# Performance work log

Hardware: AMD Instinct MI355X
Metric: run time of the kernel (lower is better)

Reference implementation:

```python
import jax, jax.numpy as jnp
import numpy as np

B, S, H, HEADS = 4, 4096, 256, 4
DH = H // HEADS
WINDOW = 16
N = B * S
EPS = 1e-5


def _build_edges():
    half = WINDOW // 2
    i = np.arange(S)
    offs = np.concatenate([np.arange(-half, 0), np.arange(1, half)])  # j in [i-half, i+half), j != i
    j = i[:, None] + offs[None, :]
    valid = (j >= 0) & (j < S)
    src_i = np.broadcast_to(i[:, None], j.shape)[valid]
    tgt_j = j[valid]
    w = (1.0 / (1.0 + np.abs(src_i - tgt_j))).astype(np.float32)
    boff = np.arange(B)[:, None] * S
    src = (boff + src_i[None, :]).reshape(-1).astype(np.int32)
    tgt = (boff + tgt_j[None, :]).reshape(-1).astype(np.int32)
    w = np.tile(w, B)
    return src, tgt, w


def setup_inputs() -> dict:
    key = jax.random.key(0)
    ks = jax.random.split(key, 8)
    src, tgt, w = _build_edges()
    sc = 0.02
    return {
        "hidden_states": jax.random.normal(ks[0], (B, S, H), jnp.float32),
        "Wc": jax.random.normal(ks[1], (H, H), jnp.float32) * sc,
        "bc": jnp.zeros((H,), jnp.float32),
        "Wa": jax.random.normal(ks[2], (H, H), jnp.float32) * sc,
        "a_src": jax.random.normal(ks[3], (HEADS, DH), jnp.float32) * sc,
        "a_tgt": jax.random.normal(ks[4], (HEADS, DH), jnp.float32) * sc,
        "ba": jnp.zeros((H,), jnp.float32),
        "ln_g": jnp.ones((H,), jnp.float32),
        "ln_b": jnp.zeros((H,), jnp.float32),
        "Wg": jax.random.normal(ks[5], (2 * H, H), jnp.float32) * sc,
        "bg": jnp.zeros((H,), jnp.float32),
        "Wp": jax.random.normal(ks[6], (H, H), jnp.float32) * sc,
        "bp": jnp.zeros((H,), jnp.float32),
        "edge_weights": jnp.asarray(w),
        "src": jnp.asarray(src),
        "tgt": jnp.asarray(tgt),
    }


def _ln(x, g, b):
    mu = jnp.mean(x, -1, keepdims=True)
    var = jnp.mean((x - mu) ** 2, -1, keepdims=True)
    return (x - mu) * jax.lax.rsqrt(var + EPS) * g + b


def reference(hidden_states, Wc, bc, Wa, a_src, a_tgt, ba, ln_g, ln_b,
              Wg, bg, Wp, bp, edge_weights, src, tgt):
    x = hidden_states.reshape(N, H)

    # --- layer 0: GraphConvolution ---
    support = x @ Wc                                   # [N,H]
    msg = edge_weights[:, None] * support[src]         # [E,H]
    gs = jax.ops.segment_sum(msg, tgt, num_segments=N) + bc
    gs = _ln(gs + x, ln_g, ln_b)

    # --- layer 1: GraphAttention (GAT-style, edge-weighted softmax) ---
    h = (gs @ Wa).reshape(N, HEADS, DH)
    es = jnp.einsum('nhd,hd->nh', h, a_src)            # [N,heads]
    et = jnp.einsum('nhd,hd->nh', h, a_tgt)
    logits = jax.nn.leaky_relu(es[src] + et[tgt], 0.2)  # [E,heads]
    m = jax.ops.segment_max(logits, tgt, num_segments=N)
    un = jnp.exp(logits - m[tgt]) * edge_weights[:, None]
    den = jax.ops.segment_sum(un, tgt, num_segments=N)
    alpha = un / (den[tgt] + 1e-9)                      # [E,heads]
    agg = jax.ops.segment_sum(alpha[:, :, None] * h[src], tgt, num_segments=N)
    gs = agg.reshape(N, H) + ba
    gs = _ln(gs + x, ln_g, ln_b)

    # --- gated integration ---
    gate = jax.nn.sigmoid(jnp.concatenate([x, gs], -1) @ Wg + bg)
    enhanced = x + gate * (gs @ Wp + bp)
    return enhanced.reshape(B, S, H)
```

## Files before the change

kernel.cpp:

```cpp
#include <hip/hip_runtime.h>
#include <math.h>

#define HD 256
#define SEQ 4096
#define NR 16384
#define NHEADS 4
#define EPSV 1e-5f
#define LDP 72
#define ZLDP 264
#define SROWS 32
#define SHALO 15
#define SLDP 264

typedef __attribute__((ext_vector_type(8))) short bf16x8;
typedef __attribute__((ext_vector_type(4))) float f32x4;

__device__ inline short f2bf(float f) {
    unsigned u = __float_as_uint(f);
    u += 0x7FFF + ((u >> 16) & 1);
    return (short)(u >> 16);
}
__device__ inline float bf2f(short s) {
    return __uint_as_float(((unsigned)(unsigned short)s) << 16);
}

__device__ inline void stage_w(const short* __restrict__ src, int src_stride,
                               int k0, short* lds)
{
    int t = threadIdx.x;
#pragma unroll
    for (int c = 0; c < 8; ++c) {
        int idx = c * 256 + t;
        int r = idx >> 3, kg = idx & 7;
        bf16x8 v = *(const bf16x8*)(src + (size_t)r * src_stride + k0 + kg * 8);
        *(bf16x8*)(lds + r * LDP + kg * 8) = v;
    }
}

__global__ __launch_bounds__(256) void prep_stencil(
    const float* __restrict__ x,
    const float* __restrict__ Wc, const float* __restrict__ Wa,
    const float* __restrict__ Wg, const float* __restrict__ Wp,
    short* __restrict__ xb, short* __restrict__ y,
    short* __restrict__ WcT, short* __restrict__ WaT,
    short* __restrict__ WgT, short* __restrict__ WpT)
{
    __shared__ __align__(16) char smem[(SROWS + SHALO) * SLDP * 2];
    int task = blockIdx.y;
    int bx = blockIdx.x;
    int t = threadIdx.x;

    if (task == 0) {
        short* lH = (short*)smem;
        int t0 = bx * SROWS;
        int batch_base = t0 & ~(SEQ - 1);
        for (int i = t; i < (SROWS + SHALO) * 64; i += 256) {
            int r = i >> 6, c4 = (i & 63) * 4;
            int grow = t0 - 7 + r;
            short4 o4 = {0, 0, 0, 0};
            if (grow >= batch_base && grow < batch_base + SEQ) {
                float4 v = *(const float4*)(x + (size_t)grow * HD + c4);
                o4.x = f2bf(v.x); o4.y = f2bf(v.y); o4.z = f2bf(v.z); o4.w = f2bf(v.w);
            }
            *(short4*)(lH + r * SLDP + c4) = o4;
        }
        __syncthreads();
        for (int i = t; i < SROWS * 64; i += 256) {
            int r = i >> 6, c4 = (i & 63) * 4;
            *(short4*)(xb + (size_t)(t0 + r) * HD + c4) =
                *(const short4*)(lH + (r + 7) * SLDP + c4);
        }
        int wv = t >> 6, lane = t & 63;
        int c0 = lane * 4;
        for (int rr = wv; rr < SROWS; rr += 4) {
            float a0 = 0.f, a1 = 0.f, a2 = 0.f, a3 = 0.f;
#pragma unroll
            for (int i = 0; i < 15; ++i) {
                int d = (i < 7) ? (i - 7) : (i - 6);
                float wd = 1.f / (1.f + (float)((d < 0) ? -d : d));
                short4 s4 = *(const short4*)(lH + (rr + 7 + d) * SLDP + c0);
                a0 += wd * bf2f(s4.x); a1 += wd * bf2f(s4.y);
                a2 += wd * bf2f(s4.z); a3 += wd * bf2f(s4.w);
            }
            short4 o;
            o.x = f2bf(a0); o.y = f2bf(a1); o.z = f2bf(a2); o.w = f2bf(a3);
            *(short4*)(y + (size_t)(t0 + rr) * HD + c0) = o;
        }
        return;
    }
    float (*lds)[65] = (float (*)[65])smem;
    const float* W; short* Wt; int K;
    if (task == 1)      { W = Wc; Wt = WcT; K = 256; }
    else if (task == 2) { W = Wa; Wt = WaT; K = 256; }
    else if (task == 3) { W = Wg; Wt = WgT; K = 512; }
    else                { W = Wp; Wt = WpT; K = 256; }
    int ntiles = (K >> 6) * 4;
    if (bx >= ntiles) return;
    int k0 = (bx >> 2) * 64, n0 = (bx & 3) * 64;
    int ty = t >> 6, tx = t & 63;
#pragma unroll
    for (int s = 0; s < 16; ++s) {
        int r = s * 4 + ty;
        lds[r][tx] = W[(size_t)(k0 + r) * 256 + n0 + tx];
    }
    __syncthreads();
#pragma unroll
    for (int s = 0; s < 16; ++s) {
        int rn = s * 4 + ty;
        Wt[(size_t)(n0 + rn) * K + k0 + tx] = f2bf(lds[tx][rn]);
    }
}

__global__ __launch_bounds__(256) void gemm_fused(
    const short* __restrict__ y, const short* __restrict__ WcT,
    const short* __restrict__ xb, const float* __restrict__ bc,
    const short* __restrict__ WaT,
    const float* __restrict__ lng, const float* __restrict__ lnb,
    const float* __restrict__ a_src, const float* __restrict__ a_tgt,
    short* __restrict__ hb, float* __restrict__ es, float* __restrict__ et)
{
    __shared__ __align__(16) short lB[256 * LDP];
    __shared__ __align__(16) short lZ[32 * ZLDP];
    __shared__ float red_s[64], red_q[64];
    int t = threadIdx.x;
    int m0 = blockIdx.x * SROWS;
    int lane = t & 63, wid = t >> 6;
    int wm = wid & 1, wn = wid >> 1;
    int lm = lane & 15, lk = (lane >> 4) * 8;
    int rbase = (lane >> 4) * 4;

#pragma unroll
    for (int c = 0; c < 4; ++c) {
        int idx = c * 256 + t;
        int r = idx >> 5, kg = idx & 31;
        *(bf16x8*)(lZ + r * ZLDP + kg * 8) =
            *(const bf16x8*)(y + (size_t)(m0 + r) * HD + kg * 8);
    }

    f32x4 acc[8] = {};
    for (int kt = 0; kt < 4; ++kt) {
        __syncthreads();
        stage_w(WcT, HD, kt * 64, lB);
        __syncthreads();
#pragma unroll
        for (int kk2 = 0; kk2 < 64; kk2 += 32) {
            bf16x8 a = *(const bf16x8*)(lZ + (wm * 16 + lm) * ZLDP + kt * 64 + kk2 + lk);
#pragma unroll
            for (int j = 0; j < 8; ++j) {
                bf16x8 b = *(const bf16x8*)(lB + (wn * 128 + j * 16 + lm) * LDP + kk2 + lk);
                acc[j] = __builtin_amdgcn_mfma_f32_16x16x32_bf16(a, b, acc[j], 0, 0, 0);
            }
        }
    }
    float zv[8][4];
    float s4r[4] = {}, q4r[4] = {};
#pragma unroll
    for (int j = 0; j < 8; ++j)
#pragma unroll
        for (int r = 0; r < 4; ++r) {
            int n = wn * 128 + j * 16 + lm;
            int row = m0 + wm * 16 + rbase + r;
            float z = acc[j][r] + bc[n] + bf2f(xb[(size_t)row * HD + n]);
            zv[j][r] = z; s4r[r] += z; q4r[r] += z * z;
        }
#pragma unroll
    for (int r = 0; r < 4; ++r)
#pragma unroll
        for (int o = 1; o < 16; o <<= 1) {
            s4r[r] += __shfl_xor(s4r[r], o, 64);
            q4r[r] += __shfl_xor(q4r[r], o, 64);
        }
    if (lm == 0)
#pragma unroll
        for (int r = 0; r < 4; ++r) {
            red_s[wn * 32 + wm * 16 + rbase + r] = s4r[r];
            red_q[wn * 32 + wm * 16 + rbase + r] = q4r[r];
        }
    __syncthreads();
    float mu[4], inv[4];
#pragma unroll
    for (int r = 0; r < 4; ++r) {
        int rowl = wm * 16 + rbase + r;
        float S = red_s[rowl] + red_s[32 + rowl];
        float Q = red_q[rowl] + red_q[32 + rowl];
        mu[r] = S * (1.f / HD);
        inv[r] = rsqrtf(Q * (1.f / HD) - mu[r] * mu[r] + EPSV);
    }
#pragma unroll
    for (int j = 0; j < 8; ++j)
#pragma unroll
        for (int r = 0; r < 4; ++r) {
            int n = wn * 128 + j * 16 + lm;
            int rowl = wm * 16 + rbase + r;
            lZ[rowl * ZLDP + n] = f2bf((zv[j][r] - mu[r]) * inv[r] * lng[n] + lnb[n]);
        }

    f32x4 acc2[8] = {};
    for (int kt = 0; kt < 4; ++kt) {
        __syncthreads();
        stage_w(WaT, HD, kt * 64, lB);
        __syncthreads();
#pragma unroll
        for (int kk2 = 0; kk2 < 64; kk2 += 32) {
            bf16x8 a = *(const bf16x8*)(lZ + (wm * 16 + lm) * ZLDP + kt * 64 + kk2 + lk);
#pragma unroll
            for (int j = 0; j < 8; ++j) {
                bf16x8 b = *(const bf16x8*)(lB + (wn * 128 + j * 16 + lm) * LDP + kk2 + lk);
                acc2[j] = __builtin_amdgcn_mfma_f32_16x16x32_bf16(a, b, acc2[j], 0, 0, 0);
            }
        }
    }
    float esA[4] = {}, etA[4] = {}, esB[4] = {}, etB[4] = {};
#pragma unroll
    for (int j = 0; j < 8; ++j) {
        int n = wn * 128 + j * 16 + lm;
        float as = a_src[n], at = a_tgt[n];
#pragma unroll
        for (int r = 0; r < 4; ++r) {
            int row = m0 + wm * 16 + rbase + r;
            hb[(size_t)row * HD + n] = f2bf(acc2[j][r]);
            if (j < 4) { esA[r] += acc2[j][r] * as; etA[r] += acc2[j][r] * at; }
            else       { esB[r] += acc2[j][r] * as; etB[r] += acc2[j][r] * at; }
        }
    }
#pragma unroll
    for (int r = 0; r < 4; ++r) {
#pragma unroll
        for (int o = 1; o < 16; o <<= 1) {
            esA[r] += __shfl_xor(esA[r], o, 64);
            etA[r] += __shfl_xor(etA[r], o, 64);
            esB[r] += __shfl_xor(esB[r], o, 64);
            etB[r] += __shfl_xor(etB[r], o, 64);
        }
        if (lm == 0) {
            int row = m0 + wm * 16 + rbase + r;
            es[row * NHEADS + wn * 2 + 0] = esA[r];
            et[row * NHEADS + wn * 2 + 0] = etA[r];
            es[row * NHEADS + wn * 2 + 1] = esB[r];
            et[row * NHEADS + wn * 2 + 1] = etB[r];
        }
    }
}

#define AF_LZ_OFF (256 * LDP * 2)
#define AF_LX_OFF (256 * LDP * 2 + 32 * ZLDP * 2)

__global__ __launch_bounds__(256) void attn_final(
    const short* __restrict__ hb, const float* __restrict__ es,
    const float* __restrict__ et, const short* __restrict__ xb,
    const float* __restrict__ ba, const float* __restrict__ lng,
    const float* __restrict__ lnb,
    const short* __restrict__ WgT, const float* __restrict__ bg,
    const short* __restrict__ WpT, const float* __restrict__ bp,
    float* __restrict__ out)
{
    __shared__ __align__(16) char smem[256 * LDP * 2 + 2 * 32 * ZLDP * 2];
    short* lH = (short*)smem;
    short* lB = (short*)smem;
    short* lZ = (short*)(smem + AF_LZ_OFF);
    short* lX = (short*)(smem + AF_LX_OFF);

    int t = threadIdx.x;
    int t0 = blockIdx.x * SROWS;
    int batch_base = t0 & ~(SEQ - 1);

    for (int i = t; i < (SROWS + SHALO) * 64; i += 256) {
        int r = i >> 6, c4 = (i & 63) * 4;
        int grow = t0 - 7 + r;
        short4 v = {0, 0, 0, 0};
        if (grow >= batch_base && grow < batch_base + SEQ)
            v = *(const short4*)(hb + (size_t)grow * HD + c4);
        *(short4*)(lH + r * SLDP + c4) = v;
    }
    for (int i = t; i < SROWS * 64; i += 256) {
        int r = i >> 6, c4 = (i & 63) * 4;
        *(short4*)(lX + r * ZLDP + c4) = *(const short4*)(xb + (size_t)(t0 + r) * HD + c4);
    }
    __syncthreads();

    int wv = t >> 6, lane = t & 63;
    int tap = lane >> 2, hh = lane & 3;
    int hd = lane >> 4;
    int c0 = lane * 4;
    for (int rr = wv; rr < SROWS; rr += 4) {
        int trow = t0 + rr;
        int p = trow & (SEQ - 1);
        float lg = -1e30f, wd = 0.f;
        bool okk = false;
        if (tap < 15) {
            int d = (tap < 7) ? (tap - 7) : (tap - 6);
            int qp = p + d;
            okk = (qp >= 0) && (qp < SEQ);
            if (okk) {
                float l = es[(trow + d) * NHEADS + hh] + et[trow * NHEADS + hh];
                lg = (l > 0.f) ? l : 0.2f * l;
            }
            wd = 1.f / (1.f + (float)((d < 0) ? -d : d));
        }
        float m = lg;
#pragma unroll
        for (int o = 4; o < 64; o <<= 1) m = fmaxf(m, __shfl_xor(m, o, 64));
        float un = okk ? __expf(lg - m) * wd : 0.f;
        float den = un;
#pragma unroll
        for (int o = 4; o < 64; o <<= 1) den += __shfl_xor(den, o, 64);
        float alpha_l = un / (den + 1e-9f);

        float al[15];
#pragma unroll
        for (int i = 0; i < 15; ++i) al[i] = __shfl(alpha_l, i * 4 + hd, 64);

        float a0 = 0.f, a1 = 0.f, a2 = 0.f, a3 = 0.f;
#pragma unroll
        for (int i = 0; i < 15; ++i) {
            int d = (i < 7) ? (i - 7) : (i - 6);
            short4 s4 = *(const short4*)(lH + (rr + 7 + d) * SLDP + c0);
            a0 += al[i] * bf2f(s4.x); a1 += al[i] * bf2f(s4.y);
            a2 += al[i] * bf2f(s4.z); a3 += al[i] * bf2f(s4.w);
        }
        short4 xv4 = *(const short4*)(lX + rr * ZLDP + c0);
        float4 bav = *(const float4*)(ba + c0);
        float v0 = a0 + bav.x + bf2f(xv4.x), v1 = a1 + bav.y + bf2f(xv4.y);
        float v2 = a2 + bav.z + bf2f(xv4.z), v3 = a3 + bav.w + bf2f(xv4.w);
        float s = v0 + v1 + v2 + v3;
        float q = v0 * v0 + v1 * v1 + v2 * v2 + v3 * v3;
#pragma unroll
        for (int o = 1; o < 64; o <<= 1) { s += __shfl_xor(s, o, 64); q += __shfl_xor(q, o, 64); }
        float mu = s * (1.f / HD);
        float var = q * (1.f / HD) - mu * mu;
        float inv = rsqrtf(var + EPSV);
        float4 gv = *(const float4*)(lng + c0);
        float4 bv = *(const float4*)(lnb + c0);
        short4 o4;
        o4.x = f2bf((v0 - mu) * inv * gv.x + bv.x);
        o4.y = f2bf((v1 - mu) * inv * gv.y + bv.y);
        o4.z = f2bf((v2 - mu) * inv * gv.z + bv.z);
        o4.w = f2bf((v3 - mu) * inv * gv.w + bv.w);
        *(short4*)(lZ + rr * ZLDP + c0) = o4;
    }

    int wid = t >> 6;
    int wm = wid & 1, wn = wid >> 1;
    int lm = lane & 15, lk = (lane >> 4) * 8;
    int rbase = (lane >> 4) * 4;
    f32x4 accg[8] = {}, accp[8] = {};
    for (int kt = 0; kt < 4; ++kt) {
        __syncthreads();
        stage_w(WgT, 512, kt * 64, lB);
        __syncthreads();
#pragma unroll
        for (int kk2 = 0; kk2 < 64; kk2 += 32) {
            bf16x8 a = *(const bf16x8*)(lX + (wm * 16 + lm) * ZLDP + kt * 64 + kk2 + lk);
#pragma unroll
            for (int j = 0; j < 8; ++j) {
                bf16x8 b = *(const bf16x8*)(lB + (wn * 128 + j * 16 + lm) * LDP + kk2 + lk);
                accg[j] = __builtin_amdgcn_mfma_f32_16x16x32_bf16(a, b, accg[j], 0, 0, 0);
            }
        }
    }
    for (int kt = 0; kt < 4; ++kt) {
        __syncthreads();
        stage_w(WgT, 512, 256 + kt * 64, lB);
        __syncthreads();
#pragma unroll
        for (int kk2 = 0; kk2 < 64; kk2 += 32) {
            bf16x8 a = *(const bf16x8*)(lZ + (wm * 16 + lm) * ZLDP + kt * 64 + kk2 + lk);
#pragma unroll
            for (int j = 0; j < 8; ++j) {
                bf16x8 b = *(const bf16x8*)(lB + (wn * 128 + j * 16 + lm) * LDP + kk2 + lk);
                accg[j] = __builtin_amdgcn_mfma_f32_16x16x32_bf16(a, b, accg[j], 0, 0, 0);
            }
        }
    }
    for (int kt = 0; kt < 4; ++kt) {
        __syncthreads();
        stage_w(WpT, HD, kt * 64, lB);
        __syncthreads();
#pragma unroll
        for (int kk2 = 0; kk2 < 64; kk2 += 32) {
            bf16x8 a = *(const bf16x8*)(lZ + (wm * 16 + lm) * ZLDP + kt * 64 + kk2 + lk);
#pragma unroll
            for (int j = 0; j < 8; ++j) {
                bf16x8 b = *(const bf16x8*)(lB + (wn * 128 + j * 16 + lm) * LDP + kk2 + lk);
                accp[j] = __builtin_amdgcn_mfma_f32_16x16x32_bf16(a, b, accp[j], 0, 0, 0);
            }
        }
    }
#pragma unroll
    for (int j = 0; j < 8; ++j)
#pragma unroll
        for (int r = 0; r < 4; ++r) {
            int n = wn * 128 + j * 16 + lm;
            int rowl = wm * 16 + rbase + r;
            size_t m = (size_t)(t0 + rowl);
            float gate = 1.f / (1.f + __expf(-(accg[j][r] + bg[n])));
            float pv = accp[j][r] + bp[n];
            out[m * HD + n] = bf2f(lX[rowl * ZLDP + n]) + gate * pv;
        }
}

extern "C" void kernel_launch(void* const* d_in, const int* in_sizes, int n_in,
                              void* d_out, int out_size, void* d_ws, size_t ws_size,
                              hipStream_t stream)
{
    const float* x     = (const float*)d_in[0];
    const float* Wc    = (const float*)d_in[1];
    const float* bc    = (const float*)d_in[2];
    const float* Wa    = (const float*)d_in[3];
    const float* a_src = (const float*)d_in[4];
    const float* a_tgt = (const float*)d_in[5];
    const float* ba    = (const float*)d_in[6];
    const float* ln_g  = (const float*)d_in[7];
    const float* ln_b  = (const float*)d_in[8];
    const float* Wg    = (const float*)d_in[9];
    const float* bg    = (const float*)d_in[10];
    const float* Wp    = (const float*)d_in[11];
    const float* bp    = (const float*)d_in[12];

    float* out = (float*)d_out;

    char* w = (char*)d_ws;
    short* y   = (short*)w;   w += (size_t)NR * HD * 2;
    short* xb  = (short*)w;   w += (size_t)NR * HD * 2;
    short* hb  = (short*)w;   w += (size_t)NR * HD * 2;
    float* es  = (float*)w;   w += (size_t)NR * NHEADS * 4;
    float* et  = (float*)w;   w += (size_t)NR * NHEADS * 4;
    short* WcT = (short*)w;   w += 256 * 256 * 2;
    short* WaT = (short*)w;   w += 256 * 256 * 2;
    short* WpT = (short*)w;   w += 256 * 256 * 2;
    short* WgT = (short*)w;   w += 512 * 256 * 2;

    prep_stencil<<<dim3(NR / SROWS, 5), 256, 0, stream>>>(
        x, Wc, Wa, Wg, Wp, xb, y, WcT, WaT, WgT, WpT);
    gemm_fused<<<NR / SROWS, 256, 0, stream>>>(y, WcT, xb, bc, WaT, ln_g, ln_b,
                                               a_src, a_tgt, hb, es, et);
    attn_final<<<NR / SROWS, 256, 0, stream>>>(hb, es, et, xb, ba, ln_g, ln_b,
                                               WgT, bg, WpT, bp, out);
}
```

Before: 67.54 us.

## Double-buffer weight tiles through registers with single barrier per k-step

Replaces the load-sync-compute-sync staging of weight tiles with a double-buffered pipeline over 32-wide k-slices. The next slice is prefetched into registers before the current MFMAs run, then stored to the alternate LDS buffer, so only one barrier is needed per step. Launch bounds gain occupancy hints (3 and 4 blocks per CU) to help hide latency. The costs are twice as many k-iterations, more registers held for the prefetch, and possible spilling under the tighter register limits.

```diff
diff --git a/kernel.cpp b/kernel.cpp
--- a/kernel.cpp
+++ b/kernel.cpp
@@ -6,7 +6,7 @@
 #define NR 16384
 #define NHEADS 4
 #define EPSV 1e-5f
-#define LDP 72
+#define LDP2 36
 #define ZLDP 264
 #define SROWS 32
 #define SHALO 15
@@ -24,16 +24,25 @@
     return __uint_as_float(((unsigned)(unsigned short)s) << 16);
 }
 
-__device__ inline void stage_w(const short* __restrict__ src, int src_stride,
-                               int k0, short* lds)
+__device__ inline void wload(const short* __restrict__ src, int src_stride,
+                             int k0, bf16x8 wreg[4])
 {
     int t = threadIdx.x;
 #pragma unroll
-    for (int c = 0; c < 8; ++c) {
+    for (int c = 0; c < 4; ++c) {
         int idx = c * 256 + t;
-        int r = idx >> 3, kg = idx & 7;
-        bf16x8 v = *(const bf16x8*)(src + (size_t)r * src_stride + k0 + kg * 8);
-        *(bf16x8*)(lds + r * LDP + kg * 8) = v;
+        int r = idx >> 2, kg = idx & 3;
+        wreg[c] = *(const bf16x8*)(src + (size_t)r * src_stride + k0 + kg * 8);
+    }
+}
+__device__ inline void wstore(short* lds, bf16x8 wreg[4])
+{
+    int t = threadIdx.x;
+#pragma unroll
+    for (int c = 0; c < 4; ++c) {
+        int idx = c * 256 + t;
+        int r = idx >> 2, kg = idx & 3;
+        *(bf16x8*)(lds + r * LDP2 + kg * 8) = wreg[c];
     }
 }
 
@@ -111,7 +120,7 @@
     }
 }
 
-__global__ __launch_bounds__(256) void gemm_fused(
+__global__ __launch_bounds__(256, 3) void gemm_fused(
     const short* __restrict__ y, const short* __restrict__ WcT,
     const short* __restrict__ xb, const float* __restrict__ bc,
     const short* __restrict__ WaT,
@@ -119,7 +128,7 @@
     const float* __restrict__ a_src, const float* __restrict__ a_tgt,
     short* __restrict__ hb, float* __restrict__ es, float* __restrict__ et)
 {
-    __shared__ __align__(16) short lB[256 * LDP];
+    __shared__ __align__(16) short lBp[2][256 * LDP2];
     __shared__ __align__(16) short lZ[32 * ZLDP];
     __shared__ float red_s[64], red_q[64];
     int t = threadIdx.x;
@@ -138,19 +147,25 @@
     }
 
     f32x4 acc[8] = {};
-    for (int kt = 0; kt < 4; ++kt) {
-        __syncthreads();
-        stage_w(WcT, HD, kt * 64, lB);
-        __syncthreads();
-#pragma unroll
-        for (int kk2 = 0; kk2 < 64; kk2 += 32) {
-            bf16x8 a = *(const bf16x8*)(lZ + (wm * 16 + lm) * ZLDP + kt * 64 + kk2 + lk);
-#pragma unroll
-            for (int j = 0; j < 8; ++j) {
-                bf16x8 b = *(const bf16x8*)(lB + (wn * 128 + j * 16 + lm) * LDP + kk2 + lk);
-                acc[j] = __builtin_amdgcn_mfma_f32_16x16x32_bf16(a, b, acc[j], 0, 0, 0);
-            }
-        }
+    {
+        bf16x8 w0[4];
+        wload(WcT, HD, 0, w0);
+        wstore(lBp[0], w0);
+    }
+    __syncthreads();
+    for (int kt = 0; kt < 8; ++kt) {
+        const short* cur = lBp[kt & 1];
+        short* nxt = (short*)lBp[(kt & 1) ^ 1];
+        bf16x8 wreg[4];
+        if (kt < 7) wload(WcT, HD, (kt + 1) * 32, wreg);
+        bf16x8 a = *(const bf16x8*)(lZ + (wm * 16 + lm) * ZLDP + kt * 32 + lk);
+#pragma unroll
+        for (int j = 0; j < 8; ++j) {
+            bf16x8 b = *(const bf16x8*)(cur + (wn * 128 + j * 16 + lm) * LDP2 + lk);
+            acc[j] = __builtin_amdgcn_mfma_f32_16x16x32_bf16(a, b, acc[j], 0, 0, 0);
+        }
+        if (kt < 7) wstore(nxt, wreg);
+        __syncthreads();
     }
     float zv[8][4];
     float s4r[4] = {}, q4r[4] = {};
@@ -194,21 +209,27 @@
             int rowl = wm * 16 + rbase + r;
             lZ[rowl * ZLDP + n] = f2bf((zv[j][r] - mu[r]) * inv[r] * lng[n] + lnb[n]);
         }
+    {
+        bf16x8 w0[4];
+        wload(WaT, HD, 0, w0);
+        wstore((short*)lBp[0], w0);
+    }
+    __syncthreads();
 
     f32x4 acc2[8] = {};
-    for (int kt = 0; kt < 4; ++kt) {
-        __syncthreads();
-        stage_w(WaT, HD, kt * 64, lB);
-        __syncthreads();
-#pragma unroll
-        for (int kk2 = 0; kk2 < 64; kk2 += 32) {
-            bf16x8 a = *(const bf16x8*)(lZ + (wm * 16 + lm) * ZLDP + kt * 64 + kk2 + lk);
-#pragma unroll
-            for (int j = 0; j < 8; ++j) {
-                bf16x8 b = *(const bf16x8*)(lB + (wn * 128 + j * 16 + lm) * LDP + kk2 + lk);
-                acc2[j] = __builtin_amdgcn_mfma_f32_16x16x32_bf16(a, b, acc2[j], 0, 0, 0);
-            }
-        }
+    for (int kt = 0; kt < 8; ++kt) {
+        const short* cur = lBp[kt & 1];
+        short* nxt = (short*)lBp[(kt & 1) ^ 1];
+        bf16x8 wreg[4];
+        if (kt < 7) wload(WaT, HD, (kt + 1) * 32, wreg);
+        bf16x8 a = *(const bf16x8*)(lZ + (wm * 16 + lm) * ZLDP + kt * 32 + lk);
+#pragma unroll
+        for (int j = 0; j < 8; ++j) {
+            bf16x8 b = *(const bf16x8*)(cur + (wn * 128 + j * 16 + lm) * LDP2 + lk);
+            acc2[j] = __builtin_amdgcn_mfma_f32_16x16x32_bf16(a, b, acc2[j], 0, 0, 0);
+        }
+        if (kt < 7) wstore(nxt, wreg);
+        __syncthreads();
     }
     float esA[4] = {}, etA[4] = {}, esB[4] = {}, etB[4] = {};
 #pragma unroll
@@ -242,10 +263,10 @@
     }
 }
 
-#define AF_LZ_OFF (256 * LDP * 2)
-#define AF_LX_OFF (256 * LDP * 2 + 32 * ZLDP * 2)
-
-__global__ __launch_bounds__(256) void attn_final(
+#define AF_LZ_OFF 36864
+#define AF_LX_OFF (36864 + 32 * ZLDP * 2)
+
+__global__ __launch_bounds__(256, 4) void attn_final(
     const short* __restrict__ hb, const float* __restrict__ es,
     const float* __restrict__ et, const short* __restrict__ xb,
     const float* __restrict__ ba, const float* __restrict__ lng,
@@ -254,11 +275,12 @@
     const short* __restrict__ WpT, const float* __restrict__ bp,
     float* __restrict__ out)
 {
-    __shared__ __align__(16) char smem[256 * LDP * 2 + 2 * 32 * ZLDP * 2];
-    short* lH = (short*)smem;
-    short* lB = (short*)smem;
-    short* lZ = (short*)(smem + AF_LZ_OFF);
-    short* lX = (short*)(smem + AF_LX_OFF);
+    __shared__ __align__(16) char smem[36864 + 2 * 32 * ZLDP * 2];
+    short* lH  = (short*)smem;
+    short* lB0 = (short*)smem;
+    short* lB1 = (short*)(smem + 256 * LDP2 * 2);
+    short* lZ  = (short*)(smem + AF_LZ_OFF);
+    short* lX  = (short*)(smem + AF_LX_OFF);
 
     int t = threadIdx.x;
     int t0 = blockIdx.x * SROWS;
@@ -338,53 +360,71 @@
         o4.w = f2bf((v3 - mu) * inv * gv.w + bv.w);
         *(short4*)(lZ + rr * ZLDP + c0) = o4;
     }
+    __syncthreads();
 
     int wid = t >> 6;
     int wm = wid & 1, wn = wid >> 1;
     int lm = lane & 15, lk = (lane >> 4) * 8;
     int rbase = (lane >> 4) * 4;
     f32x4 accg[8] = {}, accp[8] = {};
-    for (int kt = 0; kt < 4; ++kt) {
-        __syncthreads();
-        stage_w(WgT, 512, kt * 64, lB);
-        __syncthreads();
-#pragma unroll
-        for (int kk2 = 0; kk2 < 64; kk2 += 32) {
-            bf16x8 a = *(const bf16x8*)(lX + (wm * 16 + lm) * ZLDP + kt * 64 + kk2 + lk);
-#pragma unroll
-            for (int j = 0; j < 8; ++j) {
-                bf16x8 b = *(const bf16x8*)(lB + (wn * 128 + j * 16 + lm) * LDP + kk2 + lk);
-                accg[j] = __builtin_amdgcn_mfma_f32_16x16x32_bf16(a, b, accg[j], 0, 0, 0);
-            }
-        }
-    }
-    for (int kt = 0; kt < 4; ++kt) {
-        __syncthreads();
-        stage_w(WgT, 512, 256 + kt * 64, lB);
-        __syncthreads();
-#pragma unroll
-        for (int kk2 = 0; kk2 < 64; kk2 += 32) {
-            bf16x8 a = *(const bf16x8*)(lZ + (wm * 16 + lm) * ZLDP + kt * 64 + kk2 + lk);
-#pragma unroll
-            for (int j = 0; j < 8; ++j) {
-                bf16x8 b = *(const bf16x8*)(lB + (wn * 128 + j * 16 + lm) * LDP + kk2 + lk);
-                accg[j] = __builtin_amdgcn_mfma_f32_16x16x32_bf16(a, b, accg[j], 0, 0, 0);
-            }
-        }
-    }
-    for (int kt = 0; kt < 4; ++kt) {
-        __syncthreads();
-        stage_w(WpT, HD, kt * 64, lB);
-        __syncthreads();
-#pragma unroll
-        for (int kk2 = 0; kk2 < 64; kk2 += 32) {
-            bf16x8 a = *(const bf16x8*)(lZ + (wm * 16 + lm) * ZLDP + kt * 64 + kk2 + lk);
-#pragma unroll
-            for (int j = 0; j < 8; ++j) {
-                bf16x8 b = *(const bf16x8*)(lB + (wn * 128 + j * 16 + lm) * LDP + kk2 + lk);
-                accp[j] = __builtin_amdgcn_mfma_f32_16x16x32_bf16(a, b, accp[j], 0, 0, 0);
-            }
-        }
+    short* lBp[2] = {lB0, lB1};
+
+    {
+        bf16x8 w0[4];
+        wload(WgT, 512, 0, w0); wstore(lB0, w0);
+    }
+    __syncthreads();
+    for (int kt = 0; kt < 8; ++kt) {
+        const short* cur = lBp[kt & 1];
+        short* nxt = lBp[(kt & 1) ^ 1];
+        bf16x8 wreg[4];
+        if (kt < 7) wload(WgT, 512, (kt + 1) * 32, wreg);
+        bf16x8 a = *(const bf16x8*)(lX + (wm * 16 + lm) * ZLDP + kt * 32 + lk);
+#pragma unroll
+        for (int j = 0; j < 8; ++j) {
+            bf16x8 b = *(const bf16x8*)(cur + (wn * 128 + j * 16 + lm) * LDP2 + lk);
+            accg[j] = __builtin_amdgcn_mfma_f32_16x16x32_bf16(a, b, accg[j], 0, 0, 0);
+        }
+        if (kt < 7) wstore(nxt, wreg);
+        __syncthreads();
+    }
+    {
+        bf16x8 w0[4];
+        wload(WgT, 512, 256, w0); wstore(lB0, w0);
+    }
+    __syncthreads();
+    for (int kt = 0; kt < 8; ++kt) {
+        const short* cur = lBp[kt & 1];
+        short* nxt = lBp[(kt & 1) ^ 1];
+        bf16x8 wreg[4];
+        if (kt < 7) wload(WgT, 512, 256 + (kt + 1) * 32, wreg);
+        bf16x8 a = *(const bf16x8*)(lZ + (wm * 16 + lm) * ZLDP + kt * 32 + lk);
+#pragma unroll
+        for (int j = 0; j < 8; ++j) {
+            bf16x8 b = *(const bf16x8*)(cur + (wn * 128 + j * 16 + lm) * LDP2 + lk);
+            accg[j] = __builtin_amdgcn_mfma_f32_16x16x32_bf16(a, b, accg[j], 0, 0, 0);
+        }
+        if (kt < 7) wstore(nxt, wreg);
+        __syncthreads();
+    }
+    {
+        bf16x8 w0[4];
+        wload(WpT, HD, 0, w0); wstore(lB0, w0);
+    }
+    __syncthreads();
+    for (int kt = 0; kt < 8; ++kt) {
+        const short* cur = lBp[kt & 1];
+        short* nxt = lBp[(kt & 1) ^ 1];
+        bf16x8 wreg[4];
+        if (kt < 7) wload(WpT, HD, (kt + 1) * 32, wreg);
+        bf16x8 a = *(const bf16x8*)(lZ + (wm * 16 + lm) * ZLDP + kt * 32 + lk);
+#pragma unroll
+        for (int j = 0; j < 8; ++j) {
+            bf16x8 b = *(const bf16x8*)(cur + (wn * 128 + j * 16 + lm) * LDP2 + lk);
+            accp[j] = __builtin_amdgcn_mfma_f32_16x16x32_bf16(a, b, accp[j], 0, 0, 0);
+        }
+        if (kt < 7) wstore(nxt, wreg);
+        __syncthreads();
     }
 #pragma unroll
     for (int j = 0; j < 8; ++j)
```

New measurement: 151.5 us. 124% more time.
